# Performance work log

Hardware: AMD Instinct MI355X
Metric: run time of the kernel (lower is better)

Reference implementation:

```python
import jax, jax.numpy as jnp
import numpy as np

NUM_HEADS = 8


def setup_inputs() -> dict:
    key = jax.random.key(0)
    B, T, N, C = 16, 24, 716, 256
    H = NUM_HEADS
    D = C // H
    ks = jax.random.split(key, 14)

    def w(k, shape, scale=0.02):
        return jax.random.normal(k, shape, dtype=jnp.float32) * scale

    return {
        "x": jax.random.normal(ks[0], (B, T, N, C), dtype=jnp.float32),
        # nn.Linear weights stored PyTorch-style [out, in]
        "Wq": w(ks[1], (C, C)), "bq": w(ks[2], (C,)),
        "Wk": w(ks[3], (C, C)), "bk": w(ks[4], (C,)),
        "Wv": w(ks[5], (C, C)), "bv": w(ks[6], (C,)),
        "Wo": w(ks[7], (C, C)), "bo": w(ks[8], (C,)),
        # grouped conv1d (kernel_size=1) weights, squeezed: [out_ch, in_ch_per_group]
        "w1": w(ks[9], (C, D)), "b1": w(ks[10], (C,)),
        "w2": w(ks[11], (3 * C, D)), "b2": w(ks[12], (3 * C,)),
    }


def reference(x, Wq, bq, Wk, bk, Wv, bv, Wo, bo, w1, b1, w2, b2):
    B, T, N, C = x.shape
    H = NUM_HEADS
    D = C // H
    BT = B * T
    scale = D ** -0.5

    xf = x.reshape(BT, N, C)
    # q, k, v: [BT, H, N, D]
    q = (xf @ Wq.T + bq).reshape(BT, N, H, D).transpose(0, 2, 1, 3)
    k = (xf @ Wk.T + bk).reshape(BT, N, H, D).transpose(0, 2, 1, 3)
    v = (xf @ Wv.T + bv).reshape(BT, N, H, D).transpose(0, 2, 1, 3)

    # linear attention: kv outer-product [BT, H, D, D], scaled by (scale/N)
    kv = jnp.einsum('bhnd,bhne->bhde', k, v) * (scale / N)
    attn = jnp.einsum('bhnd,bhde->bhne', q, kv)
    # mean-pooled correction term
    kmean = k.mean(axis=2)  # [BT, H, D]
    vmean = v.mean(axis=2)  # [BT, H, D]
    qk = jnp.einsum('bhnd,bhd->bhn', q, kmean) * scale  # [BT, H, N]
    xa = attn + (1.0 - qk)[..., None] * vmean[:, :, None, :]
    xa = xa.transpose(0, 2, 1, 3).reshape(BT, N, C)

    # dynamic per-channel 3-tap kernel weights from node-mean features
    m = xf.mean(axis=1).reshape(BT, H, D)  # grouped input [BT, H, D]
    h1 = jnp.einsum('bgi,goi->bgo', m, w1.reshape(H, D, D)) + b1.reshape(H, D)
    h1 = jax.nn.gelu(h1, approximate=False)
    h2 = jnp.einsum('bgi,goi->bgo', h1, w2.reshape(H, 3 * D, D)) + b2.reshape(H, 3 * D)
    rw = h2.reshape(BT, C, 3)  # per-(sample, channel) 3-tap kernel

    # depthwise conv1d over node axis with groups = BT*C (cross-correlation)
    vc = v.transpose(0, 1, 3, 2).reshape(BT, C, N)
    vp = jnp.pad(vc, ((0, 0), (0, 0), (1, 1)))
    res = (rw[:, :, 0:1] * vp[:, :, 0:N]
           + rw[:, :, 1:2] * vp[:, :, 1:N + 1]
           + rw[:, :, 2:3] * vp[:, :, 2:N + 2])  # [BT, C, N]

    out = (xa + res.transpose(0, 2, 1)).reshape(B, T, N, C)
    return out @ Wo.T + bo
```

## Files before the change

kernel.cpp:

```cpp
#include <hip/hip_runtime.h>
#include <hip/hip_bf16.h>
#include <math.h>

typedef __attribute__((ext_vector_type(8))) short short8;
typedef __attribute__((ext_vector_type(4))) short sv4;
typedef __attribute__((ext_vector_type(4))) float f32x4;
typedef unsigned int u32;

#define BT_ 384
#define N_ 716
#define C_ 256
#define H_ 8
#define D_ 32
#define MROWS (BT_ * N_)
#define SCALE_ 0.17677669529663687f
#define INVN_ (1.0f / 716.0f)

__device__ __forceinline__ void gload_lds16(const void* g, void* l) {
    __builtin_amdgcn_global_load_lds(
        (const __attribute__((address_space(1))) u32*)g,
        (__attribute__((address_space(3))) u32*)l, 16, 0, 0);
}

__global__ void prep_weights(const float* __restrict__ Wq, const float* __restrict__ bq,
                             const float* __restrict__ Wk, const float* __restrict__ bk,
                             const float* __restrict__ Wv, const float* __restrict__ bv,
                             const float* __restrict__ Wo,
                             __hip_bfloat16* __restrict__ wqkv, float* __restrict__ bqkv,
                             __hip_bfloat16* __restrict__ wo) {
    int idx = blockIdx.x * 256 + threadIdx.x;
    if (idx < 768 * 256) {
        int o = idx >> 8, c = idx & 255;
        const float* W = (o < 256) ? Wq : ((o < 512) ? Wk : Wv);
        int oo = o & 255;
        wqkv[idx] = __float2bfloat16(W[oo * 256 + c]);
    }
    if (idx < 256 * 256) wo[idx] = __float2bfloat16(Wo[idx]);
    if (idx < 768) bqkv[idx] = (idx < 256) ? bq[idx] : ((idx < 512) ? bk[idx - 256] : bv[idx - 512]);
}

__global__ __launch_bounds__(256)
void convert_x(const float* __restrict__ x, __hip_bfloat16* __restrict__ xb,
               float* __restrict__ msum) {
    int bt = blockIdx.x, chunk = blockIdx.y;
    int t = threadIdx.x;
    int c4 = (t & 63) * 4;
    int r0 = t >> 6;
    size_t base = ((size_t)bt * N_ + (size_t)chunk * 179) * C_;
    float s0 = 0.f, s1 = 0.f, s2 = 0.f, s3 = 0.f;
    for (int r = r0; r < 179; r += 4) {
        float4 f = *(const float4*)&x[base + (size_t)r * C_ + c4];
        union { sv4 v; __hip_bfloat16 h[4]; } u;
        u.h[0] = __float2bfloat16(f.x);
        u.h[1] = __float2bfloat16(f.y);
        u.h[2] = __float2bfloat16(f.z);
        u.h[3] = __float2bfloat16(f.w);
        *(sv4*)&xb[base + (size_t)r * C_ + c4] = u.v;
        s0 += f.x; s1 += f.y; s2 += f.z; s3 += f.w;
    }
    atomicAdd(&msum[bt * C_ + c4 + 0], s0);
    atomicAdd(&msum[bt * C_ + c4 + 1], s1);
    atomicAdd(&msum[bt * C_ + c4 + 2], s2);
    atomicAdd(&msum[bt * C_ + c4 + 3], s3);
}

__global__ __launch_bounds__(256)
void mlp_rw(const float* __restrict__ msum, const float* __restrict__ w1,
            const float* __restrict__ b1, const float* __restrict__ w2,
            const float* __restrict__ b2, float* __restrict__ rw) {
    int bt = blockIdx.x;
    int t = threadIdx.x;
    __shared__ float m_l[256];
    __shared__ float h1_l[256];
    m_l[t] = msum[bt * 256 + t] * INVN_;
    __syncthreads();
    int g = t >> 5;
    float a = b1[t];
    #pragma unroll
    for (int i = 0; i < 32; ++i) a += m_l[g * 32 + i] * w1[t * 32 + i];
    h1_l[t] = 0.5f * a * (1.0f + erff(a * 0.70710678118654752f));
    __syncthreads();
    for (int o = t; o < 768; o += 256) {
        int gg = o / 96;
        float s = b2[o];
        #pragma unroll
        for (int i = 0; i < 32; ++i) s += h1_l[gg * 32 + i] * w2[o * 32 + i];
        rw[bt * 768 + o] = s;
    }
}

template<int NCOLS, int GRIDX, bool OUT_BF16>
__global__ __launch_bounds__(256, 2)
void gemm_persist(const __hip_bfloat16* __restrict__ A, const __hip_bfloat16* __restrict__ Bm,
                  const float* __restrict__ bias, void* __restrict__ outp) {
    __shared__ __align__(16) __hip_bfloat16 As[2][64 * 256];
    constexpr int NT = MROWS / 64;
    const int L = blockIdx.x;
    const int xcd = L & 7, w = L >> 3;
    const int cb = w % GRIDX;
    const int ib = xcd * 32 + w / GRIDX;
    const int tid = threadIdx.x;
    const int lane = tid & 63;
    const int wave = tid >> 6;
    const int wn = wave;
    const int colBase = cb * 128;
    const int l15 = lane & 15, lq = lane >> 4;
    const int lrow2 = lane >> 5;
    const int p = lane & 31;

    auto stageA = [&](int rt, int buf) {
        #pragma unroll
        for (int i = 0; i < 8; ++i) {
            int r = wave * 16 + 2 * i + lrow2;
            const __hip_bfloat16* g = A + ((size_t)rt * 64 + r) * 256 + ((p ^ (r & 7)) * 8);
            gload_lds16(g, &As[buf][(wave * 16 + 2 * i) * 256]);
        }
    };

    stageA(ib, 0);

    short8 bf[2][8];
    #pragma unroll
    for (int n = 0; n < 2; ++n)
        #pragma unroll
        for (int ks = 0; ks < 8; ++ks)
            bf[n][ks] = *(const short8*)&Bm[(size_t)(colBase + wn * 32 + n * 16 + l15) * 256 + ks * 32 + lq * 8];
    float biasr[2];
    #pragma unroll
    for (int n = 0; n < 2; ++n)
        biasr[n] = bias[colBase + wn * 32 + n * 16 + l15];

    asm volatile("s_waitcnt vmcnt(0)" ::: "memory");
    __builtin_amdgcn_s_barrier();

    int buf = 0;
    for (int rt = ib; rt < NT; rt += 256) {
        int rtn = rt + 256;
        if (rtn < NT) stageA(rtn, buf ^ 1);

        f32x4 acc[4][2] = {};
        #pragma unroll
        for (int ks = 0; ks < 8; ++ks) {
            short8 af[4];
            #pragma unroll
            for (int m = 0; m < 4; ++m) {
                int row = m * 16 + l15;
                af[m] = *(const short8*)&As[buf][row * 256 + (((ks * 4 + lq) ^ (row & 7)) * 8)];
            }
            #pragma unroll
            for (int m = 0; m < 4; ++m)
                #pragma unroll
                for (int n = 0; n < 2; ++n)
                    acc[m][n] = __builtin_amdgcn_mfma_f32_16x16x32_bf16(af[m], bf[n][ks], acc[m][n], 0, 0, 0);
        }
        asm volatile("s_waitcnt lgkmcnt(0)" ::: "memory");
        __builtin_amdgcn_s_barrier();

        if constexpr (OUT_BF16) {
            __hip_bfloat16* Cs = &As[buf][0];
            #pragma unroll
            for (int m = 0; m < 4; ++m)
                #pragma unroll
                for (int n = 0; n < 2; ++n) {
                    int col = wn * 32 + n * 16 + l15;
                    #pragma unroll
                    for (int j = 0; j < 4; ++j)
                        Cs[(m * 16 + lq * 4 + j) * 136 + col] =
                            __float2bfloat16(acc[m][n][j] + biasr[n]);
                }
            asm volatile("s_waitcnt lgkmcnt(0)" ::: "memory");
            __builtin_amdgcn_s_barrier();
            int row = tid >> 2, cq = tid & 3;
            __hip_bfloat16* og = (__hip_bfloat16*)outp + ((size_t)rt * 64 + row) * NCOLS + colBase;
            #pragma unroll
            for (int i = 0; i < 4; ++i) {
                int col = cq * 8 + i * 32;
                *(short8*)&og[col] = *(const short8*)&Cs[row * 136 + col];
            }
        } else {
            float* Cs = (float*)&As[buf][0];
            #pragma unroll
            for (int pp = 0; pp < 2; ++pp) {
                #pragma unroll
                for (int mm = 0; mm < 2; ++mm) {
                    int m = 2 * pp + mm;
                    #pragma unroll
                    for (int n = 0; n < 2; ++n) {
                        int col = wn * 32 + n * 16 + l15;
                        #pragma unroll
                        for (int j = 0; j < 4; ++j)
                            Cs[(mm * 16 + lq * 4 + j) * 132 + col] = acc[m][n][j] + biasr[n];
                    }
                }
                asm volatile("s_waitcnt lgkmcnt(0)" ::: "memory");
                __builtin_amdgcn_s_barrier();
                int row = tid >> 3, k = tid & 7;
                float* og = (float*)outp + ((size_t)rt * 64 + pp * 32 + row) * NCOLS + colBase;
                #pragma unroll
                for (int i = 0; i < 4; ++i) {
                    int col = k * 4 + i * 32;
                    *(float4*)&og[col] = *(const float4*)&Cs[row * 132 + col];
                }
                asm volatile("s_waitcnt lgkmcnt(0)" ::: "memory");
                __builtin_amdgcn_s_barrier();
            }
        }
        asm volatile("s_waitcnt vmcnt(4) lgkmcnt(0)" ::: "memory");
        __builtin_amdgcn_s_barrier();
        buf ^= 1;
    }
}

__global__ __launch_bounds__(512, 2)
void reduce_kv(const __hip_bfloat16* __restrict__ qkv, __hip_bfloat16* __restrict__ kv2t,
               float* __restrict__ vmeanb) {
    __shared__ __align__(16) __hip_bfloat16 T[512 * 64];
    const int bt = blockIdx.x;
    const int tid = threadIdx.x;
    const int lane = tid & 63;
    const int h = tid >> 6;
    const int l15 = lane & 15, lq = lane >> 4;
    const int co = tid >> 3;
    const int np3 = tid & 7;
    const size_t rowbase = (size_t)bt * N_;

    union S8 { short8 v; unsigned short u[8]; };
    const short8 zero8 = {0, 0, 0, 0, 0, 0, 0, 0};

    auto issue_loads = [&](int n0, S8* A, S8* B) {
        #pragma unroll
        for (int s = 0; s < 4; ++s) {
            int n = n0 + 2 * (np3 + 8 * s);
            A[s].v = (n < N_)     ? *(const short8*)&qkv[(rowbase + n) * 768 + 256 + co * 8] : zero8;
            B[s].v = (n + 1 < N_) ? *(const short8*)&qkv[(rowbase + n + 1) * 768 + 256 + co * 8] : zero8;
        }
    };
    auto write_lds = [&](S8* A, S8* B) {
        #pragma unroll
        for (int s = 0; s < 4; ++s) {
            int r = 2 * (np3 + 8 * s);
            int slotbase = ((r >> 3));
            #pragma unroll
            for (int j = 0; j < 8; ++j) {
                int c = co * 8 + j;
                u32 w = (u32)A[s].u[j] | ((u32)B[s].u[j] << 16);
                int off = c * 64 + ((slotbase ^ (c & 7)) << 3) + (r & 7);
                *(u32*)&T[off] = w;
            }
        }
    };

    S8 bufA[4], bufB[4], nxtA[4], nxtB[4];
    issue_loads(0, bufA, bufB);

    f32x4 acc[2][2] = {};
    f32x4 acck[2] = {};
    f32x4 accv[2] = {};
    S8 ones;
    #pragma unroll
    for (int j = 0; j < 8; ++j) ones.u[j] = 0x3F80;

    for (int chunk = 0; chunk < 12; ++chunk) {
        if (chunk < 11) issue_loads((chunk + 1) * 64, nxtA, nxtB);
        write_lds(bufA, bufB);
        __syncthreads();
        #pragma unroll
        for (int nc = 0; nc < 2; ++nc) {
            short8 af[2], bf[2];
            int slot = nc * 4 + lq;
            #pragma unroll
            for (int dh = 0; dh < 2; ++dh) {
                int c = h * 32 + dh * 16 + l15;
                af[dh] = *(const short8*)&T[c * 64 + ((slot ^ (c & 7)) << 3)];
            }
            #pragma unroll
            for (int eh = 0; eh < 2; ++eh) {
                int c = 256 + h * 32 + eh * 16 + l15;
                bf[eh] = *(const short8*)&T[c * 64 + ((slot ^ (c & 7)) << 3)];
            }
            #pragma unroll
            for (int dh = 0; dh < 2; ++dh)
                #pragma unroll
                for (int eh = 0; eh < 2; ++eh)
                    acc[dh][eh] = __builtin_amdgcn_mfma_f32_16x16x32_bf16(af[dh], bf[eh], acc[dh][eh], 0, 0, 0);
            #pragma unroll
            for (int dh = 0; dh < 2; ++dh)
                acck[dh] = __builtin_amdgcn_mfma_f32_16x16x32_bf16(af[dh], ones.v, acck[dh], 0, 0, 0);
            #pragma unroll
            for (int eh = 0; eh < 2; ++eh)
                accv[eh] = __builtin_amdgcn_mfma_f32_16x16x32_bf16(ones.v, bf[eh], accv[eh], 0, 0, 0);
        }
        __syncthreads();
        #pragma unroll
        for (int s = 0; s < 4; ++s) { bufA[s] = nxtA[s]; bufB[s] = nxtB[s]; }
    }

    const int bh = bt * 8 + h;
    #pragma unroll
    for (int eh = 0; eh < 2; ++eh) {
        int e = eh * 16 + l15;
        float vme = accv[eh][0] * INVN_;
        #pragma unroll
        for (int dh = 0; dh < 2; ++dh) {
            union { sv4 v; __hip_bfloat16 x[4]; } o;
            #pragma unroll
            for (int j = 0; j < 4; ++j) {
                float km = acck[dh][j] * INVN_;
                float val = acc[dh][eh][j] * (SCALE_ * INVN_) - SCALE_ * km * vme;
                o.x[j] = __float2bfloat16(val);
            }
            *(sv4*)&kv2t[(size_t)bh * 1024 + e * 32 + dh * 16 + lq * 4] = o.v;
        }
        if (lq == 0) vmeanb[bh * 32 + e] = vme;
    }
}

__global__ __launch_bounds__(256)
void fuse_z2(const __hip_bfloat16* __restrict__ qkv, const __hip_bfloat16* __restrict__ kv2t,
             const float* __restrict__ vmeanb, const float* __restrict__ rw,
             __hip_bfloat16* __restrict__ Z) {
    __shared__ __align__(16) __hip_bfloat16 attn[64][256];
    __shared__ __align__(16) __hip_bfloat16 kvl[8192];
    int bt = blockIdx.x;
    int n0 = blockIdx.y * 64;
    int rows = (N_ - n0 < 64) ? (N_ - n0) : 64;
    int t = threadIdx.x;
    const size_t rowbase = (size_t)bt * N_;

    {
        const __hip_bfloat16* src = kv2t + (size_t)bt * 8192;
        #pragma unroll
        for (int i = 0; i < 4; ++i) {
            int off = (t + i * 256) * 8;
            *(short8*)&kvl[off] = *(const short8*)&src[off];
        }
    }
    __syncthreads();

    {
        int lane = t & 63, wave = t >> 6;
        int l15 = lane & 15, lq = lane >> 4;
        int r0 = wave * 16;
        int gn = n0 + r0 + l15; if (gn > N_ - 1) gn = N_ - 1;
        const __hip_bfloat16* qrow = qkv + (rowbase + gn) * 768;
        #pragma unroll
        for (int h = 0; h < 8; ++h) {
            short8 af = *(const short8*)&qrow[h * 32 + lq * 8];
            #pragma unroll
            for (int half = 0; half < 2; ++half) {
                short8 bfr = *(const short8*)&kvl[h * 1024 + (half * 16 + l15) * 32 + lq * 8];
                f32x4 acc = {};
                acc = __builtin_amdgcn_mfma_f32_16x16x32_bf16(af, bfr, acc, 0, 0, 0);
                int col = h * 32 + half * 16 + l15;
                float vm = vmeanb[bt * 256 + col];
                #pragma unroll
                for (int j = 0; j < 4; ++j)
                    attn[r0 + lq * 4 + j][col] = __float2bfloat16(acc[j] + vm);
            }
        }
    }
    __syncthreads();

    {
        int tr = t >> 5;
        int c8 = (t & 31) * 8;
        float w0[8], w1_[8], w2_[8];
        #pragma unroll
        for (int u = 0; u < 8; ++u) {
            w0[u]  = rw[bt * 768 + (c8 + u) * 3 + 0];
            w1_[u] = rw[bt * 768 + (c8 + u) * 3 + 1];
            w2_[u] = rw[bt * 768 + (c8 + u) * 3 + 2];
        }
        int rbeg = tr * 8;
        if (rbeg < rows) {
            int rend = rbeg + 8; if (rend > rows) rend = rows;
            union U8 { short8 v; __hip_bfloat16 h[8]; };
            auto loadv = [&](int gn, float* dst) {
                if (gn >= 0 && gn < N_) {
                    U8 u; u.v = *(const short8*)&qkv[(rowbase + gn) * 768 + 512 + c8];
                    #pragma unroll
                    for (int uu = 0; uu < 8; ++uu) dst[uu] = __bfloat162float(u.h[uu]);
                } else {
                    #pragma unroll
                    for (int uu = 0; uu < 8; ++uu) dst[uu] = 0.0f;
                }
            };
            float vprev[8], vcur[8], vnext[8];
            loadv(n0 + rbeg - 1, vprev);
            loadv(n0 + rbeg, vcur);
            for (int r = rbeg; r < rend; ++r) {
                int gn = n0 + r;
                loadv(gn + 1, vnext);
                U8 at; at.v = *(const short8*)&attn[r][c8];
                U8 zv;
                #pragma unroll
                for (int u = 0; u < 8; ++u) {
                    float s = __bfloat162float(at.h[u]) + w0[u] * vprev[u]
                              + w1_[u] * vcur[u] + w2_[u] * vnext[u];
                    zv.h[u] = __float2bfloat16(s);
                }
                *(short8*)&Z[(rowbase + gn) * 256 + c8] = zv.v;
                #pragma unroll
                for (int u = 0; u < 8; ++u) { vprev[u] = vcur[u]; vcur[u] = vnext[u]; }
            }
        }
    }
}

extern "C" void kernel_launch(void* const* d_in, const int* in_sizes, int n_in,
                              void* d_out, int out_size, void* d_ws, size_t ws_size,
                              hipStream_t stream) {
    (void)in_sizes; (void)n_in; (void)out_size; (void)ws_size;
    const float* x  = (const float*)d_in[0];
    const float* Wq = (const float*)d_in[1];  const float* bq = (const float*)d_in[2];
    const float* Wk = (const float*)d_in[3];  const float* bk = (const float*)d_in[4];
    const float* Wv = (const float*)d_in[5];  const float* bv = (const float*)d_in[6];
    const float* Wo = (const float*)d_in[7];  const float* bo = (const float*)d_in[8];
    const float* w1 = (const float*)d_in[9];  const float* b1 = (const float*)d_in[10];
    const float* w2 = (const float*)d_in[11]; const float* b2 = (const float*)d_in[12];
    float* out = (float*)d_out;

    char* ws = (char*)d_ws;
    size_t off = 0;
    auto take = [&](size_t bytes) -> char* {
        char* p = ws + off;
        off = (off + bytes + 255) & ~(size_t)255;
        return p;
    };

    __hip_bfloat16* qkv   = (__hip_bfloat16*)take((size_t)MROWS * 768 * 2);
    __hip_bfloat16* xb    = (__hip_bfloat16*)take((size_t)MROWS * 256 * 2);
    __hip_bfloat16* Zbuf  = xb;
    __hip_bfloat16* wqkv  = (__hip_bfloat16*)take(768 * 256 * 2);
    __hip_bfloat16* wo    = (__hip_bfloat16*)take(256 * 256 * 2);
    float* bqkv   = (float*)take(768 * 4);
    float* msum   = (float*)take(384 * 256 * 4);
    float* rw     = (float*)take(384 * 768 * 4);
    __hip_bfloat16* kv2t = (__hip_bfloat16*)take((size_t)384 * 8192 * 2);
    float* vmeanb = (float*)take(384 * 256 * 4);

    hipMemsetAsync(msum, 0, 384 * 256 * 4, stream);

    prep_weights<<<768, 256, 0, stream>>>(Wq, bq, Wk, bk, Wv, bv, Wo, wqkv, bqkv, wo);
    convert_x<<<dim3(384, 4), 256, 0, stream>>>(x, xb, msum);
    mlp_rw<<<384, 256, 0, stream>>>(msum, w1, b1, w2, b2, rw);
    gemm_persist<768, 6, true><<<1536, 256, 0, stream>>>(xb, wqkv, bqkv, qkv);
    reduce_kv<<<384, 512, 0, stream>>>(qkv, kv2t, vmeanb);
    fuse_z2<<<dim3(384, 12), 256, 0, stream>>>(qkv, kv2t, vmeanb, rw, Zbuf);
    gemm_persist<256, 2, false><<<512, 256, 0, stream>>>(Zbuf, wo, bo, out);
}
```

Measured before the change: 543.8 us.

## Restructure projection GEMMs so each block computes all output columns per row tile

Replaces the templated persistent GEMM, where blocks split output columns and each reloads the same A row tile, with two dedicated kernels of 512 threads and 256 blocks. Each block now computes every output column for its 64-row tile, so A is read from global memory only once. The QKV kernel streams B fragments from global/L2 with double-buffered registers instead of holding them resident. A is staged through registers with a software prefetch two tiles ahead, replacing the direct global-to-LDS loads. The trade-offs are more register pressure, repeated B traffic through L2, and fewer blocks in flight.

```diff
diff --git a/kernel.cpp b/kernel.cpp
--- a/kernel.cpp
+++ b/kernel.cpp
@@ -13,14 +13,9 @@
 #define H_ 8
 #define D_ 32
 #define MROWS (BT_ * N_)
+#define NT_ (MROWS / 64)
 #define SCALE_ 0.17677669529663687f
 #define INVN_ (1.0f / 716.0f)
-
-__device__ __forceinline__ void gload_lds16(const void* g, void* l) {
-    __builtin_amdgcn_global_load_lds(
-        (const __attribute__((address_space(1))) u32*)g,
-        (__attribute__((address_space(3))) u32*)l, 16, 0, 0);
-}
 
 __global__ void prep_weights(const float* __restrict__ Wq, const float* __restrict__ bq,
                              const float* __restrict__ Wk, const float* __restrict__ bk,
@@ -89,125 +84,187 @@
     }
 }
 
-template<int NCOLS, int GRIDX, bool OUT_BF16>
-__global__ __launch_bounds__(256, 2)
-void gemm_persist(const __hip_bfloat16* __restrict__ A, const __hip_bfloat16* __restrict__ Bm,
-                  const float* __restrict__ bias, void* __restrict__ outp) {
-    __shared__ __align__(16) __hip_bfloat16 As[2][64 * 256];
-    constexpr int NT = MROWS / 64;
-    const int L = blockIdx.x;
-    const int xcd = L & 7, w = L >> 3;
-    const int cb = w % GRIDX;
-    const int ib = xcd * 32 + w / GRIDX;
+__global__ __launch_bounds__(512, 2)
+void gemm_qkv(const __hip_bfloat16* __restrict__ A, const __hip_bfloat16* __restrict__ Bm,
+              const float* __restrict__ bias, __hip_bfloat16* __restrict__ outp) {
+    __shared__ __align__(16) __hip_bfloat16 T[2][64 * 256];
+    __shared__ __align__(16) __hip_bfloat16 Cs[64 * 136];
+    const int bid = blockIdx.x;
     const int tid = threadIdx.x;
     const int lane = tid & 63;
-    const int wave = tid >> 6;
-    const int wn = wave;
-    const int colBase = cb * 128;
+    const int w = tid >> 6;
     const int l15 = lane & 15, lq = lane >> 4;
-    const int lrow2 = lane >> 5;
-    const int p = lane & 31;
-
-    auto stageA = [&](int rt, int buf) {
-        #pragma unroll
-        for (int i = 0; i < 8; ++i) {
-            int r = wave * 16 + 2 * i + lrow2;
-            const __hip_bfloat16* g = A + ((size_t)rt * 64 + r) * 256 + ((p ^ (r & 7)) * 8);
-            gload_lds16(g, &As[buf][(wave * 16 + 2 * i) * 256]);
-        }
-    };
-
-    stageA(ib, 0);
+    const int xr = l15 & 7;
+    const int sc = tid & 31;
+    const int rg4 = (tid >> 5) * 4;
+    const int wcol = w * 16 + l15;
+
+    short8 aload[4];
+    auto loadA4 = [&](int rt) {
+        #pragma unroll
+        for (int i = 0; i < 4; ++i)
+            aload[i] = *(const short8*)&A[((size_t)rt * 64 + rg4 + i) * 256 + sc * 8];
+    };
+    auto dsWriteA = [&](int buf) {
+        #pragma unroll
+        for (int i = 0; i < 4; ++i) {
+            int row = rg4 + i;
+            *(short8*)&T[buf][row * 256 + ((sc ^ (row & 7)) * 8)] = aload[i];
+        }
+    };
+
+    float biasr[6];
+    #pragma unroll
+    for (int c = 0; c < 6; ++c) biasr[c] = bias[c * 128 + wcol];
+
+    loadA4(bid);
+    dsWriteA(0);
+    loadA4(bid + 256);
+    asm volatile("s_waitcnt lgkmcnt(0)" ::: "memory");
+    __builtin_amdgcn_s_barrier();
+
+    int t = 0;
+    for (int rt = bid; rt < NT_; rt += 256, ++t) {
+        const int buf = t & 1;
+        if (rt + 256 < NT_) dsWriteA(buf ^ 1);
+        if (rt + 512 < NT_) loadA4(rt + 512);
+
+        const __hip_bfloat16* Tb = &T[buf][0];
+        f32x4 acc[4][6] = {};
+        short8 bfA[6], bfB[6];
+        auto loadB6 = [&](short8* dst, int ks) {
+            #pragma unroll
+            for (int c = 0; c < 6; ++c)
+                dst[c] = *(const short8*)&Bm[(size_t)(c * 128 + wcol) * 256 + ks * 32 + lq * 8];
+        };
+        auto mfma6 = [&](const short8* bfv, int ks) {
+            short8 af[4];
+            int so = ((ks * 4 + lq) ^ xr) * 8;
+            #pragma unroll
+            for (int m = 0; m < 4; ++m)
+                af[m] = *(const short8*)&Tb[(m * 16 + l15) * 256 + so];
+            #pragma unroll
+            for (int m = 0; m < 4; ++m)
+                #pragma unroll
+                for (int c = 0; c < 6; ++c)
+                    acc[m][c] = __builtin_amdgcn_mfma_f32_16x16x32_bf16(af[m], bfv[c], acc[m][c], 0, 0, 0);
+        };
+
+        loadB6(bfA, 0);
+        #pragma unroll 1
+        for (int kp = 0; kp < 4; ++kp) {
+            loadB6(bfB, kp * 2 + 1);
+            mfma6(bfA, kp * 2);
+            if (kp < 3) loadB6(bfA, kp * 2 + 2);
+            mfma6(bfB, kp * 2 + 1);
+        }
+
+        #pragma unroll 1
+        for (int c = 0; c < 6; ++c) {
+            #pragma unroll
+            for (int m = 0; m < 4; ++m)
+                #pragma unroll
+                for (int j = 0; j < 4; ++j)
+                    Cs[(m * 16 + lq * 4 + j) * 136 + wcol] =
+                        __float2bfloat16(acc[m][c][j] + biasr[c]);
+            asm volatile("s_waitcnt lgkmcnt(0)" ::: "memory");
+            __builtin_amdgcn_s_barrier();
+            int row = tid >> 3, s = tid & 7;
+            __hip_bfloat16* og = outp + ((size_t)rt * 64 + row) * 768 + c * 128 + s * 16;
+            short8 v0 = *(const short8*)&Cs[row * 136 + s * 16];
+            short8 v1 = *(const short8*)&Cs[row * 136 + s * 16 + 8];
+            *(short8*)&og[0] = v0;
+            *(short8*)&og[8] = v1;
+            __builtin_amdgcn_s_barrier();
+        }
+    }
+}
+
+__global__ __launch_bounds__(512, 2)
+void gemm_out(const __hip_bfloat16* __restrict__ A, const __hip_bfloat16* __restrict__ Bm,
+              const float* __restrict__ bias, float* __restrict__ outp) {
+    __shared__ __align__(16) __hip_bfloat16 T[2][64 * 256];
+    __shared__ __align__(16) float Csf[64 * 132];
+    const int bid = blockIdx.x;
+    const int tid = threadIdx.x;
+    const int lane = tid & 63;
+    const int w = tid >> 6;
+    const int l15 = lane & 15, lq = lane >> 4;
+    const int xr = l15 & 7;
+    const int sc = tid & 31;
+    const int rg4 = (tid >> 5) * 4;
+    const int wcol = w * 16 + l15;
+
+    short8 aload[4];
+    auto loadA4 = [&](int rt) {
+        #pragma unroll
+        for (int i = 0; i < 4; ++i)
+            aload[i] = *(const short8*)&A[((size_t)rt * 64 + rg4 + i) * 256 + sc * 8];
+    };
+    auto dsWriteA = [&](int buf) {
+        #pragma unroll
+        for (int i = 0; i < 4; ++i) {
+            int row = rg4 + i;
+            *(short8*)&T[buf][row * 256 + ((sc ^ (row & 7)) * 8)] = aload[i];
+        }
+    };
 
     short8 bf[2][8];
     #pragma unroll
-    for (int n = 0; n < 2; ++n)
+    for (int c = 0; c < 2; ++c)
         #pragma unroll
         for (int ks = 0; ks < 8; ++ks)
-            bf[n][ks] = *(const short8*)&Bm[(size_t)(colBase + wn * 32 + n * 16 + l15) * 256 + ks * 32 + lq * 8];
+            bf[c][ks] = *(const short8*)&Bm[(size_t)(c * 128 + wcol) * 256 + ks * 32 + lq * 8];
     float biasr[2];
     #pragma unroll
-    for (int n = 0; n < 2; ++n)
-        biasr[n] = bias[colBase + wn * 32 + n * 16 + l15];
-
-    asm volatile("s_waitcnt vmcnt(0)" ::: "memory");
+    for (int c = 0; c < 2; ++c) biasr[c] = bias[c * 128 + wcol];
+
+    loadA4(bid);
+    dsWriteA(0);
+    loadA4(bid + 256);
+    asm volatile("s_waitcnt lgkmcnt(0)" ::: "memory");
     __builtin_amdgcn_s_barrier();
 
-    int buf = 0;
-    for (int rt = ib; rt < NT; rt += 256) {
-        int rtn = rt + 256;
-        if (rtn < NT) stageA(rtn, buf ^ 1);
-
+    int t = 0;
+    for (int rt = bid; rt < NT_; rt += 256, ++t) {
+        const int buf = t & 1;
+        if (rt + 256 < NT_) dsWriteA(buf ^ 1);
+        if (rt + 512 < NT_) loadA4(rt + 512);
+
+        const __hip_bfloat16* Tb = &T[buf][0];
         f32x4 acc[4][2] = {};
         #pragma unroll
         for (int ks = 0; ks < 8; ++ks) {
             short8 af[4];
-            #pragma unroll
-            for (int m = 0; m < 4; ++m) {
-                int row = m * 16 + l15;
-                af[m] = *(const short8*)&As[buf][row * 256 + (((ks * 4 + lq) ^ (row & 7)) * 8)];
-            }
+            int so = ((ks * 4 + lq) ^ xr) * 8;
             #pragma unroll
             for (int m = 0; m < 4; ++m)
-                #pragma unroll
-                for (int n = 0; n < 2; ++n)
-                    acc[m][n] = __builtin_amdgcn_mfma_f32_16x16x32_bf16(af[m], bf[n][ks], acc[m][n], 0, 0, 0);
-        }
-        asm volatile("s_waitcnt lgkmcnt(0)" ::: "memory");
-        __builtin_amdgcn_s_barrier();
-
-        if constexpr (OUT_BF16) {
-            __hip_bfloat16* Cs = &As[buf][0];
+                af[m] = *(const short8*)&Tb[(m * 16 + l15) * 256 + so];
             #pragma unroll
             for (int m = 0; m < 4; ++m)
                 #pragma unroll
-                for (int n = 0; n < 2; ++n) {
-                    int col = wn * 32 + n * 16 + l15;
-                    #pragma unroll
-                    for (int j = 0; j < 4; ++j)
-                        Cs[(m * 16 + lq * 4 + j) * 136 + col] =
-                            __float2bfloat16(acc[m][n][j] + biasr[n]);
-                }
+                for (int c = 0; c < 2; ++c)
+                    acc[m][c] = __builtin_amdgcn_mfma_f32_16x16x32_bf16(af[m], bf[c][ks], acc[m][c], 0, 0, 0);
+        }
+
+        #pragma unroll 1
+        for (int c = 0; c < 2; ++c) {
+            #pragma unroll
+            for (int m = 0; m < 4; ++m)
+                #pragma unroll
+                for (int j = 0; j < 4; ++j)
+                    Csf[(m * 16 + lq * 4 + j) * 132 + wcol] = acc[m][c][j] + biasr[c];
             asm volatile("s_waitcnt lgkmcnt(0)" ::: "memory");
             __builtin_amdgcn_s_barrier();
-            int row = tid >> 2, cq = tid & 3;
-            __hip_bfloat16* og = (__hip_bfloat16*)outp + ((size_t)rt * 64 + row) * NCOLS + colBase;
+            int row = tid >> 3, s = tid & 7;
+            float* og = outp + ((size_t)rt * 64 + row) * 256 + c * 128;
             #pragma unroll
             for (int i = 0; i < 4; ++i) {
-                int col = cq * 8 + i * 32;
-                *(short8*)&og[col] = *(const short8*)&Cs[row * 136 + col];
-            }
-        } else {
-            float* Cs = (float*)&As[buf][0];
-            #pragma unroll
-            for (int pp = 0; pp < 2; ++pp) {
-                #pragma unroll
-                for (int mm = 0; mm < 2; ++mm) {
-                    int m = 2 * pp + mm;
-                    #pragma unroll
-                    for (int n = 0; n < 2; ++n) {
-                        int col = wn * 32 + n * 16 + l15;
-                        #pragma unroll
-                        for (int j = 0; j < 4; ++j)
-                            Cs[(mm * 16 + lq * 4 + j) * 132 + col] = acc[m][n][j] + biasr[n];
-                    }
-                }
-                asm volatile("s_waitcnt lgkmcnt(0)" ::: "memory");
-                __builtin_amdgcn_s_barrier();
-                int row = tid >> 3, k = tid & 7;
-                float* og = (float*)outp + ((size_t)rt * 64 + pp * 32 + row) * NCOLS + colBase;
-                #pragma unroll
-                for (int i = 0; i < 4; ++i) {
-                    int col = k * 4 + i * 32;
-                    *(float4*)&og[col] = *(const float4*)&Cs[row * 132 + col];
-                }
-                asm volatile("s_waitcnt lgkmcnt(0)" ::: "memory");
-                __builtin_amdgcn_s_barrier();
-            }
-        }
-        asm volatile("s_waitcnt vmcnt(4) lgkmcnt(0)" ::: "memory");
-        __builtin_amdgcn_s_barrier();
-        buf ^= 1;
+                int col = s * 4 + i * 32;
+                *(float4*)&og[col] = *(const float4*)&Csf[row * 132 + col];
+            }
+            __builtin_amdgcn_s_barrier();
+        }
     }
 }
 
@@ -227,15 +284,15 @@
     union S8 { short8 v; unsigned short u[8]; };
     const short8 zero8 = {0, 0, 0, 0, 0, 0, 0, 0};
 
-    auto issue_loads = [&](int n0, S8* A, S8* B) {
+    auto issue_loads = [&](int n0, S8* Aq, S8* Bq) {
         #pragma unroll
         for (int s = 0; s < 4; ++s) {
             int n = n0 + 2 * (np3 + 8 * s);
-            A[s].v = (n < N_)     ? *(const short8*)&qkv[(rowbase + n) * 768 + 256 + co * 8] : zero8;
-            B[s].v = (n + 1 < N_) ? *(const short8*)&qkv[(rowbase + n + 1) * 768 + 256 + co * 8] : zero8;
-        }
-    };
-    auto write_lds = [&](S8* A, S8* B) {
+            Aq[s].v = (n < N_)     ? *(const short8*)&qkv[(rowbase + n) * 768 + 256 + co * 8] : zero8;
+            Bq[s].v = (n + 1 < N_) ? *(const short8*)&qkv[(rowbase + n + 1) * 768 + 256 + co * 8] : zero8;
+        }
+    };
+    auto write_lds = [&](S8* Aq, S8* Bq) {
         #pragma unroll
         for (int s = 0; s < 4; ++s) {
             int r = 2 * (np3 + 8 * s);
@@ -243,9 +300,9 @@
             #pragma unroll
             for (int j = 0; j < 8; ++j) {
                 int c = co * 8 + j;
-                u32 w = (u32)A[s].u[j] | ((u32)B[s].u[j] << 16);
+                u32 wv = (u32)Aq[s].u[j] | ((u32)Bq[s].u[j] << 16);
                 int off = c * 64 + ((slotbase ^ (c & 7)) << 3) + (r & 7);
-                *(u32*)&T[off] = w;
+                *(u32*)&T[off] = wv;
             }
         }
     };
@@ -266,7 +323,7 @@
         __syncthreads();
         #pragma unroll
         for (int nc = 0; nc < 2; ++nc) {
-            short8 af[2], bf[2];
+            short8 af[2], bfr[2];
             int slot = nc * 4 + lq;
             #pragma unroll
             for (int dh = 0; dh < 2; ++dh) {
@@ -276,19 +333,19 @@
             #pragma unroll
             for (int eh = 0; eh < 2; ++eh) {
                 int c = 256 + h * 32 + eh * 16 + l15;
-                bf[eh] = *(const short8*)&T[c * 64 + ((slot ^ (c & 7)) << 3)];
+                bfr[eh] = *(const short8*)&T[c * 64 + ((slot ^ (c & 7)) << 3)];
             }
             #pragma unroll
             for (int dh = 0; dh < 2; ++dh)
                 #pragma unroll
                 for (int eh = 0; eh < 2; ++eh)
-                    acc[dh][eh] = __builtin_amdgcn_mfma_f32_16x16x32_bf16(af[dh], bf[eh], acc[dh][eh], 0, 0, 0);
+                    acc[dh][eh] = __builtin_amdgcn_mfma_f32_16x16x32_bf16(af[dh], bfr[eh], acc[dh][eh], 0, 0, 0);
             #pragma unroll
             for (int dh = 0; dh < 2; ++dh)
                 acck[dh] = __builtin_amdgcn_mfma_f32_16x16x32_bf16(af[dh], ones.v, acck[dh], 0, 0, 0);
             #pragma unroll
             for (int eh = 0; eh < 2; ++eh)
-                accv[eh] = __builtin_amdgcn_mfma_f32_16x16x32_bf16(ones.v, bf[eh], accv[eh], 0, 0, 0);
+                accv[eh] = __builtin_amdgcn_mfma_f32_16x16x32_bf16(ones.v, bfr[eh], accv[eh], 0, 0, 0);
         }
         __syncthreads();
         #pragma unroll
@@ -444,8 +501,8 @@
     prep_weights<<<768, 256, 0, stream>>>(Wq, bq, Wk, bk, Wv, bv, Wo, wqkv, bqkv, wo);
     convert_x<<<dim3(384, 4), 256, 0, stream>>>(x, xb, msum);
     mlp_rw<<<384, 256, 0, stream>>>(msum, w1, b1, w2, b2, rw);
-    gemm_persist<768, 6, true><<<1536, 256, 0, stream>>>(xb, wqkv, bqkv, qkv);
+    gemm_qkv<<<256, 512, 0, stream>>>(xb, wqkv, bqkv, qkv);
     reduce_kv<<<384, 512, 0, stream>>>(qkv, kv2t, vmeanb);
     fuse_z2<<<dim3(384, 12), 256, 0, stream>>>(qkv, kv2t, vmeanb, rw, Zbuf);
-    gemm_persist<256, 2, false><<<512, 256, 0, stream>>>(Zbuf, wo, bo, out);
-}
+    gemm_out<<<256, 512, 0, stream>>>(Zbuf, wo, bo, out);
+}
```

Result: slower. 1.212 ms (+122.8%).

## Single-buffer GEMM A tile, reload B fragments per tile, raise occupancy

Applied to the files above, without the earlier changes.

The persistent GEMM drops its double-buffered LDS A tile for a single buffer and stops holding all B fragments in registers, reloading them from global memory in two halves per row tile. Launch bounds go from 2 to 4 blocks per CU. The LDS-staged coalesced epilogue is replaced by direct scattered per-element global stores, and the next tile's load is issued after the MMA loop instead of overlapping it. The aim is higher occupancy to hide latency, at the cost of losing explicit prefetch overlap, repeated B loads, and uncoalesced output writes.

```diff
diff --git a/kernel.cpp b/kernel.cpp
--- a/kernel.cpp
+++ b/kernel.cpp
@@ -13,6 +13,7 @@
 #define H_ 8
 #define D_ 32
 #define MROWS (BT_ * N_)
+#define NT_ (MROWS / 64)
 #define SCALE_ 0.17677669529663687f
 #define INVN_ (1.0f / 716.0f)
 
@@ -90,11 +91,10 @@
 }
 
 template<int NCOLS, int GRIDX, bool OUT_BF16>
-__global__ __launch_bounds__(256, 2)
+__global__ __launch_bounds__(256, 4)
 void gemm_persist(const __hip_bfloat16* __restrict__ A, const __hip_bfloat16* __restrict__ Bm,
                   const float* __restrict__ bias, void* __restrict__ outp) {
-    __shared__ __align__(16) __hip_bfloat16 As[2][64 * 256];
-    constexpr int NT = MROWS / 64;
+    __shared__ __align__(16) __hip_bfloat16 As[64 * 256];
     const int L = blockIdx.x;
     const int xcd = L & 7, w = L >> 3;
     const int cb = w % GRIDX;
@@ -108,106 +108,72 @@
     const int lrow2 = lane >> 5;
     const int p = lane & 31;
 
-    auto stageA = [&](int rt, int buf) {
+    auto stageA = [&](int rt) {
         #pragma unroll
         for (int i = 0; i < 8; ++i) {
             int r = wave * 16 + 2 * i + lrow2;
             const __hip_bfloat16* g = A + ((size_t)rt * 64 + r) * 256 + ((p ^ (r & 7)) * 8);
-            gload_lds16(g, &As[buf][(wave * 16 + 2 * i) * 256]);
+            gload_lds16(g, &As[(wave * 16 + 2 * i) * 256]);
         }
     };
 
-    stageA(ib, 0);
-
-    short8 bf[2][8];
-    #pragma unroll
-    for (int n = 0; n < 2; ++n)
-        #pragma unroll
-        for (int ks = 0; ks < 8; ++ks)
-            bf[n][ks] = *(const short8*)&Bm[(size_t)(colBase + wn * 32 + n * 16 + l15) * 256 + ks * 32 + lq * 8];
+    const __hip_bfloat16* Bbase = Bm + (size_t)(colBase + wn * 32 + l15) * 256 + lq * 8;
     float biasr[2];
     #pragma unroll
     for (int n = 0; n < 2; ++n)
         biasr[n] = bias[colBase + wn * 32 + n * 16 + l15];
 
-    asm volatile("s_waitcnt vmcnt(0)" ::: "memory");
-    __builtin_amdgcn_s_barrier();
-
-    int buf = 0;
-    for (int rt = ib; rt < NT; rt += 256) {
-        int rtn = rt + 256;
-        if (rtn < NT) stageA(rtn, buf ^ 1);
+    stageA(ib);
+
+    for (int rt = ib; rt < NT_; rt += 256) {
+        asm volatile("s_waitcnt vmcnt(0)" ::: "memory");
+        __builtin_amdgcn_s_barrier();
 
         f32x4 acc[4][2] = {};
         #pragma unroll
-        for (int ks = 0; ks < 8; ++ks) {
-            short8 af[4];
-            #pragma unroll
-            for (int m = 0; m < 4; ++m) {
-                int row = m * 16 + l15;
-                af[m] = *(const short8*)&As[buf][row * 256 + (((ks * 4 + lq) ^ (row & 7)) * 8)];
-            }
-            #pragma unroll
-            for (int m = 0; m < 4; ++m)
-                #pragma unroll
-                for (int n = 0; n < 2; ++n)
-                    acc[m][n] = __builtin_amdgcn_mfma_f32_16x16x32_bf16(af[m], bf[n][ks], acc[m][n], 0, 0, 0);
+        for (int half = 0; half < 2; ++half) {
+            short8 bfr[2][4];
+            #pragma unroll
+            for (int n = 0; n < 2; ++n)
+                #pragma unroll
+                for (int k2 = 0; k2 < 4; ++k2)
+                    bfr[n][k2] = *(const short8*)(Bbase + (size_t)n * 16 * 256 + (half * 4 + k2) * 32);
+            #pragma unroll
+            for (int k2 = 0; k2 < 4; ++k2) {
+                int ks = half * 4 + k2;
+                short8 af[4];
+                #pragma unroll
+                for (int m = 0; m < 4; ++m) {
+                    int row = m * 16 + l15;
+                    af[m] = *(const short8*)&As[row * 256 + (((ks * 4 + lq) ^ (row & 7)) * 8)];
+                }
+                #pragma unroll
+                for (int m = 0; m < 4; ++m)
+                    #pragma unroll
+                    for (int n = 0; n < 2; ++n)
+                        acc[m][n] = __builtin_amdgcn_mfma_f32_16x16x32_bf16(af[m], bfr[n][k2], acc[m][n], 0, 0, 0);
+            }
         }
         asm volatile("s_waitcnt lgkmcnt(0)" ::: "memory");
         __builtin_amdgcn_s_barrier();
 
-        if constexpr (OUT_BF16) {
-            __hip_bfloat16* Cs = &As[buf][0];
-            #pragma unroll
-            for (int m = 0; m < 4; ++m)
-                #pragma unroll
-                for (int n = 0; n < 2; ++n) {
-                    int col = wn * 32 + n * 16 + l15;
-                    #pragma unroll
-                    for (int j = 0; j < 4; ++j)
-                        Cs[(m * 16 + lq * 4 + j) * 136 + col] =
-                            __float2bfloat16(acc[m][n][j] + biasr[n]);
+        if (rt + 256 < NT_) stageA(rt + 256);
+
+        #pragma unroll
+        for (int m = 0; m < 4; ++m)
+            #pragma unroll
+            for (int n = 0; n < 2; ++n) {
+                int col = colBase + wn * 32 + n * 16 + l15;
+                #pragma unroll
+                for (int j = 0; j < 4; ++j) {
+                    size_t row = (size_t)rt * 64 + m * 16 + lq * 4 + j;
+                    float val = acc[m][n][j] + biasr[n];
+                    if (OUT_BF16)
+                        ((__hip_bfloat16*)outp)[row * NCOLS + col] = __float2bfloat16(val);
+                    else
+                        ((float*)outp)[row * NCOLS + col] = val;
                 }
-            asm volatile("s_waitcnt lgkmcnt(0)" ::: "memory");
-            __builtin_amdgcn_s_barrier();
-            int row = tid >> 2, cq = tid & 3;
-            __hip_bfloat16* og = (__hip_bfloat16*)outp + ((size_t)rt * 64 + row) * NCOLS + colBase;
-            #pragma unroll
-            for (int i = 0; i < 4; ++i) {
-                int col = cq * 8 + i * 32;
-                *(short8*)&og[col] = *(const short8*)&Cs[row * 136 + col];
-            }
-        } else {
-            float* Cs = (float*)&As[buf][0];
-            #pragma unroll
-            for (int pp = 0; pp < 2; ++pp) {
-                #pragma unroll
-                for (int mm = 0; mm < 2; ++mm) {
-                    int m = 2 * pp + mm;
-                    #pragma unroll
-                    for (int n = 0; n < 2; ++n) {
-                        int col = wn * 32 + n * 16 + l15;
-                        #pragma unroll
-                        for (int j = 0; j < 4; ++j)
-                            Cs[(mm * 16 + lq * 4 + j) * 132 + col] = acc[m][n][j] + biasr[n];
-                    }
-                }
-                asm volatile("s_waitcnt lgkmcnt(0)" ::: "memory");
-                __builtin_amdgcn_s_barrier();
-                int row = tid >> 3, k = tid & 7;
-                float* og = (float*)outp + ((size_t)rt * 64 + pp * 32 + row) * NCOLS + colBase;
-                #pragma unroll
-                for (int i = 0; i < 4; ++i) {
-                    int col = k * 4 + i * 32;
-                    *(float4*)&og[col] = *(const float4*)&Cs[row * 132 + col];
-                }
-                asm volatile("s_waitcnt lgkmcnt(0)" ::: "memory");
-                __builtin_amdgcn_s_barrier();
-            }
-        }
-        asm volatile("s_waitcnt vmcnt(4) lgkmcnt(0)" ::: "memory");
-        __builtin_amdgcn_s_barrier();
-        buf ^= 1;
+            }
     }
 }
 
@@ -227,15 +193,15 @@
     union S8 { short8 v; unsigned short u[8]; };
     const short8 zero8 = {0, 0, 0, 0, 0, 0, 0, 0};
 
-    auto issue_loads = [&](int n0, S8* A, S8* B) {
+    auto issue_loads = [&](int n0, S8* Aq, S8* Bq) {
         #pragma unroll
         for (int s = 0; s < 4; ++s) {
             int n = n0 + 2 * (np3 + 8 * s);
-            A[s].v = (n < N_)     ? *(const short8*)&qkv[(rowbase + n) * 768 + 256 + co * 8] : zero8;
-            B[s].v = (n + 1 < N_) ? *(const short8*)&qkv[(rowbase + n + 1) * 768 + 256 + co * 8] : zero8;
+            Aq[s].v = (n < N_)     ? *(const short8*)&qkv[(rowbase + n) * 768 + 256 + co * 8] : zero8;
+            Bq[s].v = (n + 1 < N_) ? *(const short8*)&qkv[(rowbase + n + 1) * 768 + 256 + co * 8] : zero8;
         }
     };
-    auto write_lds = [&](S8* A, S8* B) {
+    auto write_lds = [&](S8* Aq, S8* Bq) {
         #pragma unroll
         for (int s = 0; s < 4; ++s) {
             int r = 2 * (np3 + 8 * s);
@@ -243,9 +209,9 @@
             #pragma unroll
             for (int j = 0; j < 8; ++j) {
                 int c = co * 8 + j;
-                u32 w = (u32)A[s].u[j] | ((u32)B[s].u[j] << 16);
+                u32 wv = (u32)Aq[s].u[j] | ((u32)Bq[s].u[j] << 16);
                 int off = c * 64 + ((slotbase ^ (c & 7)) << 3) + (r & 7);
-                *(u32*)&T[off] = w;
+                *(u32*)&T[off] = wv;
             }
         }
     };
@@ -266,7 +232,7 @@
         __syncthreads();
         #pragma unroll
         for (int nc = 0; nc < 2; ++nc) {
-            short8 af[2], bf[2];
+            short8 af[2], bfr[2];
             int slot = nc * 4 + lq;
             #pragma unroll
             for (int dh = 0; dh < 2; ++dh) {
@@ -276,19 +242,19 @@
             #pragma unroll
             for (int eh = 0; eh < 2; ++eh) {
                 int c = 256 + h * 32 + eh * 16 + l15;
-                bf[eh] = *(const short8*)&T[c * 64 + ((slot ^ (c & 7)) << 3)];
+                bfr[eh] = *(const short8*)&T[c * 64 + ((slot ^ (c & 7)) << 3)];
             }
             #pragma unroll
             for (int dh = 0; dh < 2; ++dh)
                 #pragma unroll
                 for (int eh = 0; eh < 2; ++eh)
-                    acc[dh][eh] = __builtin_amdgcn_mfma_f32_16x16x32_bf16(af[dh], bf[eh], acc[dh][eh], 0, 0, 0);
+                    acc[dh][eh] = __builtin_amdgcn_mfma_f32_16x16x32_bf16(af[dh], bfr[eh], acc[dh][eh], 0, 0, 0);
             #pragma unroll
             for (int dh = 0; dh < 2; ++dh)
                 acck[dh] = __builtin_amdgcn_mfma_f32_16x16x32_bf16(af[dh], ones.v, acck[dh], 0, 0, 0);
             #pragma unroll
             for (int eh = 0; eh < 2; ++eh)
-                accv[eh] = __builtin_amdgcn_mfma_f32_16x16x32_bf16(ones.v, bf[eh], accv[eh], 0, 0, 0);
+                accv[eh] = __builtin_amdgcn_mfma_f32_16x16x32_bf16(ones.v, bfr[eh], accv[eh], 0, 0, 0);
         }
         __syncthreads();
         #pragma unroll
```

New measurement: 686.8 us (median of 2 runs). +26.3%, slower.

## Use 8-wave blocks in persistent GEMM and overlap prefetch with epilogue

Applied to the files above, without the earlier changes.

The persistent GEMM block grows from 4 to 8 waves, with each wave now owning a 32x32 output sub-tile in a 2x4 wave grid instead of a 64x32 strip. This roughly halves per-wave accumulator and A-fragment registers and doubles the waves resident per CU, aiming for better latency hiding. The next A tile is now prefetched after the MFMA loop finishes, so it overlaps the epilogue rather than the compute loop. The fp32 epilogue uses a smaller 64-column staging pass, and the bf16 output path waits on its global stores before reusing LDS. Some reduce_kv variables are only renamed.

```diff
diff --git a/kernel.cpp b/kernel.cpp
--- a/kernel.cpp
+++ b/kernel.cpp
@@ -13,6 +13,7 @@
 #define H_ 8
 #define D_ 32
 #define MROWS (BT_ * N_)
+#define NT_ (MROWS / 64)
 #define SCALE_ 0.17677669529663687f
 #define INVN_ (1.0f / 716.0f)
 
@@ -90,11 +91,10 @@
 }
 
 template<int NCOLS, int GRIDX, bool OUT_BF16>
-__global__ __launch_bounds__(256, 2)
+__global__ __launch_bounds__(512, 2)
 void gemm_persist(const __hip_bfloat16* __restrict__ A, const __hip_bfloat16* __restrict__ Bm,
                   const float* __restrict__ bias, void* __restrict__ outp) {
     __shared__ __align__(16) __hip_bfloat16 As[2][64 * 256];
-    constexpr int NT = MROWS / 64;
     const int L = blockIdx.x;
     const int xcd = L & 7, w = L >> 3;
     const int cb = w % GRIDX;
@@ -102,7 +102,8 @@
     const int tid = threadIdx.x;
     const int lane = tid & 63;
     const int wave = tid >> 6;
-    const int wn = wave;
+    const int wr = wave & 1;
+    const int wc = wave >> 1;
     const int colBase = cb * 128;
     const int l15 = lane & 15, lq = lane >> 4;
     const int lrow2 = lane >> 5;
@@ -110,45 +111,41 @@
 
     auto stageA = [&](int rt, int buf) {
         #pragma unroll
-        for (int i = 0; i < 8; ++i) {
-            int r = wave * 16 + 2 * i + lrow2;
+        for (int i = 0; i < 4; ++i) {
+            int r = wave * 8 + 2 * i + lrow2;
             const __hip_bfloat16* g = A + ((size_t)rt * 64 + r) * 256 + ((p ^ (r & 7)) * 8);
-            gload_lds16(g, &As[buf][(wave * 16 + 2 * i) * 256]);
+            gload_lds16(g, &As[buf][(wave * 8 + 2 * i) * 256]);
         }
     };
-
-    stageA(ib, 0);
 
     short8 bf[2][8];
     #pragma unroll
     for (int n = 0; n < 2; ++n)
         #pragma unroll
         for (int ks = 0; ks < 8; ++ks)
-            bf[n][ks] = *(const short8*)&Bm[(size_t)(colBase + wn * 32 + n * 16 + l15) * 256 + ks * 32 + lq * 8];
+            bf[n][ks] = *(const short8*)&Bm[(size_t)(colBase + wc * 32 + n * 16 + l15) * 256 + ks * 32 + lq * 8];
     float biasr[2];
     #pragma unroll
     for (int n = 0; n < 2; ++n)
-        biasr[n] = bias[colBase + wn * 32 + n * 16 + l15];
-
+        biasr[n] = bias[colBase + wc * 32 + n * 16 + l15];
+
+    stageA(ib, 0);
     asm volatile("s_waitcnt vmcnt(0)" ::: "memory");
     __builtin_amdgcn_s_barrier();
 
     int buf = 0;
-    for (int rt = ib; rt < NT; rt += 256) {
-        int rtn = rt + 256;
-        if (rtn < NT) stageA(rtn, buf ^ 1);
-
-        f32x4 acc[4][2] = {};
+    for (int rt = ib; rt < NT_; rt += 256) {
+        f32x4 acc[2][2] = {};
         #pragma unroll
         for (int ks = 0; ks < 8; ++ks) {
-            short8 af[4];
-            #pragma unroll
-            for (int m = 0; m < 4; ++m) {
-                int row = m * 16 + l15;
+            short8 af[2];
+            #pragma unroll
+            for (int m = 0; m < 2; ++m) {
+                int row = wr * 32 + m * 16 + l15;
                 af[m] = *(const short8*)&As[buf][row * 256 + (((ks * 4 + lq) ^ (row & 7)) * 8)];
             }
             #pragma unroll
-            for (int m = 0; m < 4; ++m)
+            for (int m = 0; m < 2; ++m)
                 #pragma unroll
                 for (int n = 0; n < 2; ++n)
                     acc[m][n] = __builtin_amdgcn_mfma_f32_16x16x32_bf16(af[m], bf[n][ks], acc[m][n], 0, 0, 0);
@@ -156,57 +153,59 @@
         asm volatile("s_waitcnt lgkmcnt(0)" ::: "memory");
         __builtin_amdgcn_s_barrier();
 
+        if (rt + 256 < NT_) stageA(rt + 256, buf ^ 1);
+
         if constexpr (OUT_BF16) {
             __hip_bfloat16* Cs = &As[buf][0];
             #pragma unroll
-            for (int m = 0; m < 4; ++m)
+            for (int m = 0; m < 2; ++m)
                 #pragma unroll
                 for (int n = 0; n < 2; ++n) {
-                    int col = wn * 32 + n * 16 + l15;
+                    int col = wc * 32 + n * 16 + l15;
                     #pragma unroll
                     for (int j = 0; j < 4; ++j)
-                        Cs[(m * 16 + lq * 4 + j) * 136 + col] =
+                        Cs[(wr * 32 + m * 16 + lq * 4 + j) * 136 + col] =
                             __float2bfloat16(acc[m][n][j] + biasr[n]);
                 }
             asm volatile("s_waitcnt lgkmcnt(0)" ::: "memory");
             __builtin_amdgcn_s_barrier();
-            int row = tid >> 2, cq = tid & 3;
-            __hip_bfloat16* og = (__hip_bfloat16*)outp + ((size_t)rt * 64 + row) * NCOLS + colBase;
-            #pragma unroll
-            for (int i = 0; i < 4; ++i) {
-                int col = cq * 8 + i * 32;
-                *(short8*)&og[col] = *(const short8*)&Cs[row * 136 + col];
-            }
+            int row = tid >> 3, s = tid & 7;
+            __hip_bfloat16* og = (__hip_bfloat16*)outp + ((size_t)rt * 64 + row) * NCOLS + colBase + s * 16;
+            short8 v0 = *(const short8*)&Cs[row * 136 + s * 16];
+            short8 v1 = *(const short8*)&Cs[row * 136 + s * 16 + 8];
+            *(short8*)&og[0] = v0;
+            *(short8*)&og[8] = v1;
+            asm volatile("s_waitcnt vmcnt(2)" ::: "memory");
+            __builtin_amdgcn_s_barrier();
         } else {
             float* Cs = (float*)&As[buf][0];
             #pragma unroll
-            for (int pp = 0; pp < 2; ++pp) {
-                #pragma unroll
-                for (int mm = 0; mm < 2; ++mm) {
-                    int m = 2 * pp + mm;
+            for (int cc = 0; cc < 2; ++cc) {
+                if ((wc >> 1) == cc) {
                     #pragma unroll
-                    for (int n = 0; n < 2; ++n) {
-                        int col = wn * 32 + n * 16 + l15;
+                    for (int m = 0; m < 2; ++m)
                         #pragma unroll
-                        for (int j = 0; j < 4; ++j)
-                            Cs[(mm * 16 + lq * 4 + j) * 132 + col] = acc[m][n][j] + biasr[n];
-                    }
+                        for (int n = 0; n < 2; ++n) {
+                            int col = (wc & 1) * 32 + n * 16 + l15;
+                            #pragma unroll
+                            for (int j = 0; j < 4; ++j)
+                                Cs[(wr * 32 + m * 16 + lq * 4 + j) * 68 + col] = acc[m][n][j] + biasr[n];
+                        }
                 }
                 asm volatile("s_waitcnt lgkmcnt(0)" ::: "memory");
                 __builtin_amdgcn_s_barrier();
-                int row = tid >> 3, k = tid & 7;
-                float* og = (float*)outp + ((size_t)rt * 64 + pp * 32 + row) * NCOLS + colBase;
-                #pragma unroll
-                for (int i = 0; i < 4; ++i) {
-                    int col = k * 4 + i * 32;
-                    *(float4*)&og[col] = *(const float4*)&Cs[row * 132 + col];
+                int row = tid >> 3, s = tid & 7;
+                float* og = (float*)outp + ((size_t)rt * 64 + row) * NCOLS + colBase + cc * 64;
+                #pragma unroll
+                for (int i = 0; i < 2; ++i) {
+                    int col = s * 4 + i * 32;
+                    *(float4*)&og[col] = *(const float4*)&Cs[row * 68 + col];
                 }
-                asm volatile("s_waitcnt lgkmcnt(0)" ::: "memory");
                 __builtin_amdgcn_s_barrier();
             }
-        }
-        asm volatile("s_waitcnt vmcnt(4) lgkmcnt(0)" ::: "memory");
-        __builtin_amdgcn_s_barrier();
+            asm volatile("s_waitcnt vmcnt(4)" ::: "memory");
+            __builtin_amdgcn_s_barrier();
+        }
         buf ^= 1;
     }
 }
@@ -227,15 +226,15 @@
     union S8 { short8 v; unsigned short u[8]; };
     const short8 zero8 = {0, 0, 0, 0, 0, 0, 0, 0};
 
-    auto issue_loads = [&](int n0, S8* A, S8* B) {
+    auto issue_loads = [&](int n0, S8* Aq, S8* Bq) {
         #pragma unroll
         for (int s = 0; s < 4; ++s) {
             int n = n0 + 2 * (np3 + 8 * s);
-            A[s].v = (n < N_)     ? *(const short8*)&qkv[(rowbase + n) * 768 + 256 + co * 8] : zero8;
-            B[s].v = (n + 1 < N_) ? *(const short8*)&qkv[(rowbase + n + 1) * 768 + 256 + co * 8] : zero8;
+            Aq[s].v = (n < N_)     ? *(const short8*)&qkv[(rowbase + n) * 768 + 256 + co * 8] : zero8;
+            Bq[s].v = (n + 1 < N_) ? *(const short8*)&qkv[(rowbase + n + 1) * 768 + 256 + co * 8] : zero8;
         }
     };
-    auto write_lds = [&](S8* A, S8* B) {
+    auto write_lds = [&](S8* Aq, S8* Bq) {
         #pragma unroll
         for (int s = 0; s < 4; ++s) {
             int r = 2 * (np3 + 8 * s);
@@ -243,9 +242,9 @@
             #pragma unroll
             for (int j = 0; j < 8; ++j) {
                 int c = co * 8 + j;
-                u32 w = (u32)A[s].u[j] | ((u32)B[s].u[j] << 16);
+                u32 wv = (u32)Aq[s].u[j] | ((u32)Bq[s].u[j] << 16);
                 int off = c * 64 + ((slotbase ^ (c & 7)) << 3) + (r & 7);
-                *(u32*)&T[off] = w;
+                *(u32*)&T[off] = wv;
             }
         }
     };
@@ -266,7 +265,7 @@
         __syncthreads();
         #pragma unroll
         for (int nc = 0; nc < 2; ++nc) {
-            short8 af[2], bf[2];
+            short8 af[2], bfr[2];
             int slot = nc * 4 + lq;
             #pragma unroll
             for (int dh = 0; dh < 2; ++dh) {
@@ -276,19 +275,19 @@
             #pragma unroll
             for (int eh = 0; eh < 2; ++eh) {
                 int c = 256 + h * 32 + eh * 16 + l15;
-                bf[eh] = *(const short8*)&T[c * 64 + ((slot ^ (c & 7)) << 3)];
+                bfr[eh] = *(const short8*)&T[c * 64 + ((slot ^ (c & 7)) << 3)];
             }
             #pragma unroll
             for (int dh = 0; dh < 2; ++dh)
                 #pragma unroll
                 for (int eh = 0; eh < 2; ++eh)
-                    acc[dh][eh] = __builtin_amdgcn_mfma_f32_16x16x32_bf16(af[dh], bf[eh], acc[dh][eh], 0, 0, 0);
+                    acc[dh][eh] = __builtin_amdgcn_mfma_f32_16x16x32_bf16(af[dh], bfr[eh], acc[dh][eh], 0, 0, 0);
             #pragma unroll
             for (int dh = 0; dh < 2; ++dh)
                 acck[dh] = __builtin_amdgcn_mfma_f32_16x16x32_bf16(af[dh], ones.v, acck[dh], 0, 0, 0);
             #pragma unroll
             for (int eh = 0; eh < 2; ++eh)
-                accv[eh] = __builtin_amdgcn_mfma_f32_16x16x32_bf16(ones.v, bf[eh], accv[eh], 0, 0, 0);
+                accv[eh] = __builtin_amdgcn_mfma_f32_16x16x32_bf16(ones.v, bfr[eh], accv[eh], 0, 0, 0);
         }
         __syncthreads();
         #pragma unroll
@@ -444,8 +443,8 @@
     prep_weights<<<768, 256, 0, stream>>>(Wq, bq, Wk, bk, Wv, bv, Wo, wqkv, bqkv, wo);
     convert_x<<<dim3(384, 4), 256, 0, stream>>>(x, xb, msum);
     mlp_rw<<<384, 256, 0, stream>>>(msum, w1, b1, w2, b2, rw);
-    gemm_persist<768, 6, true><<<1536, 256, 0, stream>>>(xb, wqkv, bqkv, qkv);
+    gemm_persist<768, 6, true><<<1536, 512, 0, stream>>>(xb, wqkv, bqkv, qkv);
     reduce_kv<<<384, 512, 0, stream>>>(qkv, kv2t, vmeanb);
     fuse_z2<<<dim3(384, 12), 256, 0, stream>>>(qkv, kv2t, vmeanb, rw, Zbuf);
-    gemm_persist<256, 2, false><<<512, 256, 0, stream>>>(Zbuf, wo, bo, out);
-}
+    gemm_persist<256, 2, false><<<512, 512, 0, stream>>>(Zbuf, wo, bo, out);
+}
```

New measurement: 562.8 us. +3.5%, slower.
